# Optimization experiments

Hardware: AMD Instinct MI355X
Metric: run time of the kernel (lower is better)

Reference implementation:

```python
import jax, jax.numpy as jnp
import numpy as np

N_NODES = 10000
N_EDGES = 320000
HIDDEN = 16      # hidden_state_size
MSG = 64         # message_size
EDGE_FEAT = 32


def setup_inputs() -> dict:
    key = jax.random.key(0)
    ks = jax.random.split(key, 8)
    node_features = jax.random.normal(ks[0], (N_NODES, HIDDEN), dtype=jnp.float32)
    edge_features = jax.random.normal(ks[1], (N_EDGES, EDGE_FEAT), dtype=jnp.float32)
    edge_sources = jax.random.randint(ks[2], (N_EDGES,), 0, N_NODES, dtype=jnp.int32)
    edge_targets = jax.random.randint(ks[3], (N_EDGES,), 0, N_NODES, dtype=jnp.int32)
    hidden = jax.random.normal(ks[4], (N_NODES, HIDDEN), dtype=jnp.float32)
    initial = jax.random.normal(ks[5], (N_NODES, HIDDEN), dtype=jnp.float32)
    # Dense(edge_feat -> MSG*HIDDEN), glorot-ish scale
    W = jax.random.normal(ks[6], (EDGE_FEAT, MSG * HIDDEN), dtype=jnp.float32) / np.float32(np.sqrt(EDGE_FEAT))
    b = jnp.zeros((MSG * HIDDEN,), dtype=jnp.float32)
    return {
        "node_features": node_features,
        "edge_features": edge_features,
        "edge_sources": edge_sources,
        "edge_targets": edge_targets,
        "hidden": hidden,
        "initial": initial,
        "W": W,
        "b": b,
    }


def reference(node_features, edge_features, edge_sources, edge_targets, hidden, initial, W, b):
    # Per edge: edge_mat = Dense(edge_feat) reshaped (MSG, HIDDEN);
    # message = edge_mat @ hidden[source]; aggregate = sum over incoming edges per target node.
    num_nodes = node_features.shape[0]
    edge_mat = (edge_features @ W + b).reshape(-1, MSG, HIDDEN)  # [E, M, H]
    neigh = hidden[edge_sources]                                  # [E, H] gather
    messages = jnp.einsum("emh,eh->em", edge_mat, neigh)         # [E, M] batched matvec
    out = jax.ops.segment_sum(messages, edge_targets, num_segments=num_nodes)  # [N, M]
    return out
```

## Files before the change

### kernel.cpp

```cpp
#include <hip/hip_runtime.h>
#include <hip/hip_bf16.h>

#define N_NODES 10000
#define N_EDGES 320000
#define HIDDEN 16
#define MSG 64
#define EDGE_FEAT 32
#define KSTEPS 17
#define EPB 64

typedef __attribute__((ext_vector_type(2))) _Float16 f16x2;
typedef __attribute__((ext_vector_type(4))) _Float16 f16x4;
typedef __attribute__((ext_vector_type(8))) _Float16 f16x8;
typedef __attribute__((ext_vector_type(4))) float    f32x4;

union H8 { f16x8 v; f16x2 p[4]; f16x4 q[2]; };

__global__ void zero_prep(const float* __restrict__ W, const float* __restrict__ bias,
                          ushort* __restrict__ WrB, int* __restrict__ cnt,
                          float4* __restrict__ out4, int n4) {
    if (blockIdx.x < KSTEPS) {
        const int ks   = blockIdx.x;
        const int nt   = threadIdx.x >> 6;
        const int lane = threadIdx.x & 63;
        const int g    = lane >> 4;
        const int n    = nt * 16 + (lane & 15);
        ushort* dst = WrB + (((size_t)ks * 4 + nt) * 64 + lane) * 8;
        #pragma unroll
        for (int i = 0; i < 8; ++i) {
            const int k = ks * 32 + g * 8 + i;
            float v;
            if (k < 512)      v = W[(size_t)(k >> 4) * 1024 + n * 16 + (k & 15)];
            else if (k < 528) v = bias[n * 16 + (k - 512)];
            else              v = 0.0f;
            const _Float16 hv = (_Float16)v;
            dst[i] = *reinterpret_cast<const ushort*>(&hv);
        }
    } else if (blockIdx.x < KSTEPS + 40) {
        const int idx = (blockIdx.x - KSTEPS) * 256 + threadIdx.x;
        if (idx < N_NODES) cnt[idx] = 0;
    } else {
        const int i = (blockIdx.x - KSTEPS - 40) * 256 + threadIdx.x;
        if (i < n4) out4[i] = make_float4(0.f, 0.f, 0.f, 0.f);
    }
}

__global__ __launch_bounds__(256) void rank_kernel(const int* __restrict__ tgt,
                                                   int* __restrict__ cnt,
                                                   int* __restrict__ rank) {
    const int e = blockIdx.x * 256 + threadIdx.x;
    if (e < N_EDGES) rank[e] = atomicAdd(&cnt[tgt[e]], 1);
}

__global__ __launch_bounds__(1024) void scan_kernel(const int* __restrict__ cnt,
                                                    int* __restrict__ starts) {
    __shared__ int wsum[16];
    __shared__ int wbase[16];
    const int tid  = threadIdx.x;
    const int lane = tid & 63;
    const int wv   = tid >> 6;
    int c[10];
    int s = 0;
    #pragma unroll
    for (int j = 0; j < 10; ++j) {
        const int idx = tid * 10 + j;
        c[j] = (idx < N_NODES) ? cnt[idx] : 0;
        s += c[j];
    }
    int v = s;
    #pragma unroll
    for (int d = 1; d < 64; d <<= 1) {
        const int u = __shfl_up(v, d);
        if (lane >= d) v += u;
    }
    if (lane == 63) wsum[wv] = v;
    __syncthreads();
    if (tid < 16) {
        const int w = wsum[tid];
        int iv = w;
        #pragma unroll
        for (int d = 1; d < 16; d <<= 1) {
            const int u = __shfl_up(iv, d);
            if (tid >= d) iv += u;
        }
        wbase[tid] = iv - w;
    }
    __syncthreads();
    int running = wbase[wv] + (v - s);
    #pragma unroll
    for (int j = 0; j < 10; ++j) {
        const int idx = tid * 10 + j;
        if (idx < N_NODES) starts[idx] = running;
        running += c[j];
    }
    if (tid == 1023) starts[N_NODES] = N_EDGES;
}

__global__ __launch_bounds__(256) void build_desc(
    const int* __restrict__ tgt, const int* __restrict__ rank,
    const int* __restrict__ starts, const int* __restrict__ src,
    int4* __restrict__ edesc) {
    const int e = blockIdx.x * 256 + threadIdx.x;
    if (e < N_EDGES) {
        const int t = tgt[e];
        edesc[starts[t] + rank[e]] = make_int4(e, src[e], t, 0);
    }
}

__global__ __launch_bounds__(256, 8) void fused_msg(
    const int4*   __restrict__ edesc,
    const float*  __restrict__ ef,
    const float*  __restrict__ hidden,
    const ushort* __restrict__ WrB,
    float*        __restrict__ out)
{
    __shared__ _Float16 ef_h[EPB][36];
    __shared__ _Float16 nb_h[EPB][16];
    __shared__ int      tgt_s[EPB];
    __shared__ _Float16 msg_h[EPB][68];

    const int tid = threadIdx.x;
    const int s0  = blockIdx.x * EPB;

    {
        const int sl = tid >> 2;
        const int q  = tid & 3;
        const int4 d = edesc[s0 + sl];
        const int e  = d.x;
        const int sn = d.y;

        const float4* ep = (const float4*)(ef + (size_t)e * EDGE_FEAT + q * 8);
        const float4 v0 = ep[0], v1 = ep[1];
        _Float16* dst = &ef_h[sl][q * 8];
        *(f16x4*)(dst + 0) = f16x4{(_Float16)v0.x, (_Float16)v0.y, (_Float16)v0.z, (_Float16)v0.w};
        *(f16x4*)(dst + 4) = f16x4{(_Float16)v1.x, (_Float16)v1.y, (_Float16)v1.z, (_Float16)v1.w};

        const float4 h0 = *(const float4*)(hidden + (size_t)sn * HIDDEN + q * 4);
        *(f16x4*)&nb_h[sl][q * 4] =
            f16x4{(_Float16)h0.x, (_Float16)h0.y, (_Float16)h0.z, (_Float16)h0.w};

        if (q == 3) {
            ef_h[sl][32] = (_Float16)1.0f;
            ef_h[sl][33] = (_Float16)0.0f;
            ef_h[sl][34] = (_Float16)0.0f;
            ef_h[sl][35] = (_Float16)0.0f;
        } else if (q == 0) {
            tgt_s[sl] = d.z;
        }
    }
    __syncthreads();

    const int nt   = tid >> 6;
    const int lane = tid & 63;
    const int er   = lane & 15;
    const int g    = lane >> 4;
    const int hoff = (g & 1) * 8;
    const int fg   = g >> 1;

    H8 nb[4];
    #pragma unroll
    for (int rt = 0; rt < 4; ++rt)
        nb[rt].v = *(const f16x8*)&nb_h[rt * 16 + er][hoff];

    f32x4 acc[4];
    #pragma unroll
    for (int rt = 0; rt < 4; ++rt) acc[rt] = f32x4{0.f, 0.f, 0.f, 0.f};

    const f16x8* Bp = (const f16x8*)WrB;

    #pragma unroll
    for (int ks = 0; ks < KSTEPS; ++ks) {
        const f16x8 b = Bp[(ks * 4 + nt) * 64 + lane];
        #pragma unroll
        for (int rt = 0; rt < 4; ++rt) {
            const _Float16 a = ef_h[rt * 16 + er][2 * ks + fg];
            const f16x2 av = {a, a};
            H8 af;
            #pragma unroll
            for (int q = 0; q < 4; ++q) af.p[q] = av * nb[rt].p[q];
            acc[rt] = __builtin_amdgcn_mfma_f32_16x16x32_f16(af.v, b, acc[rt], 0, 0, 0);
        }
    }

    #pragma unroll
    for (int rt = 0; rt < 4; ++rt) {
        #pragma unroll
        for (int r = 0; r < 4; ++r) {
            msg_h[rt * 16 + g * 4 + r][nt * 16 + er] = (_Float16)acc[rt][r];
        }
    }
    __syncthreads();

    const int c = tid & 63;
    const int rbase = (tid >> 6) * 16;
    float run = (float)msg_h[rbase][c];
    int   cur = tgt_s[rbase];
    #pragma unroll
    for (int r = 1; r < 16; ++r) {
        const int   tg = tgt_s[rbase + r];
        const float m  = (float)msg_h[rbase + r][c];
        if (tg != cur) {
            atomicAdd(out + (size_t)cur * MSG + c, run);
            cur = tg;
            run = m;
        } else {
            run += m;
        }
    }
    atomicAdd(out + (size_t)cur * MSG + c, run);
}

__global__ __launch_bounds__(256) void zero_out(float* __restrict__ p, int n4) {
    const int i = blockIdx.x * 256 + threadIdx.x;
    if (i < n4) ((float4*)p)[i] = make_float4(0.f, 0.f, 0.f, 0.f);
}

__global__ __launch_bounds__(256, 4) void msg_mfma(
    const float* __restrict__ ef, const int* __restrict__ src,
    const int* __restrict__ tgt, const float* __restrict__ hidden,
    const ushort* __restrict__ WrB, float* __restrict__ out)
{
    __shared__ float ef_s[64][36];
    __shared__ float neigh_s[64][20];
    __shared__ int   tgt_s[64];
    const int tid = threadIdx.x;
    const int e0  = blockIdx.x * 64;
    {
        const int e = tid >> 2, h4 = (tid & 3) * 4;
        const int s = src[e0 + e];
        *(float4*)&neigh_s[e][h4] = *(const float4*)(hidden + (size_t)s * HIDDEN + h4);
    }
    {
        const int e = tid >> 2, f8 = (tid & 3) * 8;
        const float* p = ef + (size_t)(e0 + e) * EDGE_FEAT + f8;
        *(float4*)&ef_s[e][f8]     = *(const float4*)(p);
        *(float4*)&ef_s[e][f8 + 4] = *(const float4*)(p + 4);
    }
    if (tid < 64) { ef_s[tid][32] = 1.0f; ef_s[tid][33] = 0.0f; tgt_s[tid] = tgt[e0 + tid]; }
    __syncthreads();
    const int wave = tid >> 6, lane = tid & 63;
    const int er = lane & 15, g = lane >> 4;
    const int e_loc = wave * 16 + er;
    const int h0 = (g & 1) * 8, fg = g >> 1;
    float nb[8];
    #pragma unroll
    for (int j = 0; j < 8; ++j) nb[j] = neigh_s[e_loc][h0 + j];
    f32x4 acc0 = {0.f,0.f,0.f,0.f}, acc1 = acc0, acc2 = acc0, acc3 = acc0;
    const f16x8* Bp = (const f16x8*)WrB;
    #pragma unroll
    for (int ks = 0; ks < KSTEPS; ++ks) {
        const float a = ef_s[e_loc][2 * ks + fg];
        f16x8 af;
        #pragma unroll
        for (int j = 0; j < 8; ++j) af[j] = (_Float16)(a * nb[j]);
        const f16x8 b0 = Bp[(ks * 4 + 0) * 64 + lane];
        const f16x8 b1 = Bp[(ks * 4 + 1) * 64 + lane];
        const f16x8 b2 = Bp[(ks * 4 + 2) * 64 + lane];
        const f16x8 b3 = Bp[(ks * 4 + 3) * 64 + lane];
        acc0 = __builtin_amdgcn_mfma_f32_16x16x32_f16(af, b0, acc0, 0, 0, 0);
        acc1 = __builtin_amdgcn_mfma_f32_16x16x32_f16(af, b1, acc1, 0, 0, 0);
        acc2 = __builtin_amdgcn_mfma_f32_16x16x32_f16(af, b2, acc2, 0, 0, 0);
        acc3 = __builtin_amdgcn_mfma_f32_16x16x32_f16(af, b3, acc3, 0, 0, 0);
    }
    #pragma unroll
    for (int r = 0; r < 4; ++r) {
        const int t = tgt_s[wave * 16 + g * 4 + r];
        float* op = out + (size_t)t * MSG;
        atomicAdd(op +      er, acc0[r]);
        atomicAdd(op + 16 + er, acc1[r]);
        atomicAdd(op + 32 + er, acc2[r]);
        atomicAdd(op + 48 + er, acc3[r]);
    }
}

extern "C" void kernel_launch(void* const* d_in, const int* in_sizes, int n_in,
                              void* d_out, int out_size, void* d_ws, size_t ws_size,
                              hipStream_t stream) {
    const float* ef     = (const float*)d_in[1];
    const int*   src    = (const int*)d_in[2];
    const int*   tgt    = (const int*)d_in[3];
    const float* hidden = (const float*)d_in[4];
    const float* W      = (const float*)d_in[6];
    const float* bias   = (const float*)d_in[7];
    float* out = (float*)d_out;
    char*  ws  = (char*)d_ws;

    const size_t o_wrb    = 0;
    const size_t o_starts = 69632;
    const size_t o_cnt    = 109648;
    const size_t o_rank   = 149648;
    const size_t o_desc   = 1429648;
    const size_t need     = o_desc + (size_t)N_EDGES * 16;

    ushort* WrB = (ushort*)(ws + o_wrb);
    const int n4 = out_size / 4;

    if (ws_size >= need) {
        int*  starts = (int*)(ws + o_starts);
        int*  cnt    = (int*)(ws + o_cnt);
        int*  rank   = (int*)(ws + o_rank);
        int4* edesc  = (int4*)(ws + o_desc);

        const int zb_cnt = 40;
        const int zb_out = (n4 + 255) / 256;
        zero_prep<<<KSTEPS + zb_cnt + zb_out, 256, 0, stream>>>(W, bias, WrB, cnt,
                                                                (float4*)out, n4);
        rank_kernel<<<(N_EDGES + 255) / 256, 256, 0, stream>>>(tgt, cnt, rank);
        scan_kernel<<<1, 1024, 0, stream>>>(cnt, starts);
        build_desc<<<(N_EDGES + 255) / 256, 256, 0, stream>>>(tgt, rank, starts, src, edesc);
        fused_msg<<<N_EDGES / EPB, 256, 0, stream>>>(edesc, ef, hidden, WrB, out);
    } else {
        zero_prep<<<KSTEPS, 256, 0, stream>>>(W, bias, WrB, nullptr, nullptr, 0);
        zero_out<<<(n4 + 255) / 256, 256, 0, stream>>>(out, n4);
        msg_mfma<<<N_EDGES / 64, 256, 0, stream>>>(ef, src, tgt, hidden, WrB, out);
    }
}
```

Before: 75.68 us.

## Process two edge chunks per block with prefetch and 2x2 MFMA wave tiling

Each block of fused_msg now handles two 64-edge chunks, prefetching the next chunk's descriptors, edge features and hidden rows into registers while the current chunk computes and scatters. The MFMA work is retiled so each wave computes a 2x2 block of 16x16 tiles, which reuses the A fragments and B loads across two MFMAs each. The intent is to hide gather latency and cut redundant B-matrix loads per wave. In exchange there are half as many blocks, more registers per thread, and an extra barrier per chunk.

```diff
diff --git a/kernel.cpp b/kernel.cpp
--- a/kernel.cpp
+++ b/kernel.cpp
@@ -8,6 +8,7 @@
 #define EDGE_FEAT 32
 #define KSTEPS 17
 #define EPB 64
+#define NCHUNK 2
 
 typedef __attribute__((ext_vector_type(2))) _Float16 f16x2;
 typedef __attribute__((ext_vector_type(4))) _Float16 f16x4;
@@ -116,98 +117,114 @@
 {
     __shared__ _Float16 ef_h[EPB][36];
     __shared__ _Float16 nb_h[EPB][16];
-    __shared__ int      tgt_s[EPB];
+    __shared__ int      tgt_s[2][EPB];
     __shared__ _Float16 msg_h[EPB][68];
 
-    const int tid = threadIdx.x;
-    const int s0  = blockIdx.x * EPB;
-
-    {
-        const int sl = tid >> 2;
-        const int q  = tid & 3;
-        const int4 d = edesc[s0 + sl];
-        const int e  = d.x;
-        const int sn = d.y;
-
-        const float4* ep = (const float4*)(ef + (size_t)e * EDGE_FEAT + q * 8);
-        const float4 v0 = ep[0], v1 = ep[1];
-        _Float16* dst = &ef_h[sl][q * 8];
-        *(f16x4*)(dst + 0) = f16x4{(_Float16)v0.x, (_Float16)v0.y, (_Float16)v0.z, (_Float16)v0.w};
-        *(f16x4*)(dst + 4) = f16x4{(_Float16)v1.x, (_Float16)v1.y, (_Float16)v1.z, (_Float16)v1.w};
-
-        const float4 h0 = *(const float4*)(hidden + (size_t)sn * HIDDEN + q * 4);
-        *(f16x4*)&nb_h[sl][q * 4] =
-            f16x4{(_Float16)h0.x, (_Float16)h0.y, (_Float16)h0.z, (_Float16)h0.w};
-
-        if (q == 3) {
-            ef_h[sl][32] = (_Float16)1.0f;
-            ef_h[sl][33] = (_Float16)0.0f;
-            ef_h[sl][34] = (_Float16)0.0f;
-            ef_h[sl][35] = (_Float16)0.0f;
-        } else if (q == 0) {
-            tgt_s[sl] = d.z;
-        }
-    }
-    __syncthreads();
-
-    const int nt   = tid >> 6;
+    const int tid  = threadIdx.x;
+    const int sl   = tid >> 2;
+    const int q    = tid & 3;
+    const int base = blockIdx.x * (EPB * NCHUNK);
+
+    const int w    = tid >> 6;
+    const int wr   = w >> 1;
+    const int wc   = w & 1;
     const int lane = tid & 63;
     const int er   = lane & 15;
     const int g    = lane >> 4;
     const int hoff = (g & 1) * 8;
     const int fg   = g >> 1;
-
-    H8 nb[4];
-    #pragma unroll
-    for (int rt = 0; rt < 4; ++rt)
-        nb[rt].v = *(const f16x8*)&nb_h[rt * 16 + er][hoff];
-
-    f32x4 acc[4];
-    #pragma unroll
-    for (int rt = 0; rt < 4; ++rt) acc[rt] = f32x4{0.f, 0.f, 0.f, 0.f};
-
+    const int rt0 = wr * 2, rt1 = wr * 2 + 1;
+    const int ct0 = wc * 2, ct1 = wc * 2 + 1;
     const f16x8* Bp = (const f16x8*)WrB;
 
-    #pragma unroll
-    for (int ks = 0; ks < KSTEPS; ++ks) {
-        const f16x8 b = Bp[(ks * 4 + nt) * 64 + lane];
-        #pragma unroll
-        for (int rt = 0; rt < 4; ++rt) {
-            const _Float16 a = ef_h[rt * 16 + er][2 * ks + fg];
-            const f16x2 av = {a, a};
-            H8 af;
+    int4   d   = edesc[base + sl];
+    float4 pe0 = *(const float4*)(ef + (size_t)d.x * EDGE_FEAT + q * 8);
+    float4 pe1 = *(const float4*)(ef + (size_t)d.x * EDGE_FEAT + q * 8 + 4);
+    float4 ph  = *(const float4*)(hidden + (size_t)d.y * HIDDEN + q * 4);
+
+    #pragma unroll
+    for (int c = 0; c < NCHUNK; ++c) {
+        {
+            _Float16* dst = &ef_h[sl][q * 8];
+            *(f16x4*)(dst + 0) = f16x4{(_Float16)pe0.x, (_Float16)pe0.y,
+                                       (_Float16)pe0.z, (_Float16)pe0.w};
+            *(f16x4*)(dst + 4) = f16x4{(_Float16)pe1.x, (_Float16)pe1.y,
+                                       (_Float16)pe1.z, (_Float16)pe1.w};
+            *(f16x4*)&nb_h[sl][q * 4] = f16x4{(_Float16)ph.x, (_Float16)ph.y,
+                                              (_Float16)ph.z, (_Float16)ph.w};
+            if (q == 3) {
+                ef_h[sl][32] = (_Float16)1.0f;
+                ef_h[sl][33] = (_Float16)0.0f;
+                ef_h[sl][34] = (_Float16)0.0f;
+                ef_h[sl][35] = (_Float16)0.0f;
+            } else if (q == 0) {
+                tgt_s[c & 1][sl] = d.z;
+            }
+        }
+        __syncthreads();
+
+        if (c + 1 < NCHUNK) d = edesc[base + (c + 1) * EPB + sl];
+
+        H8 nb0, nb1;
+        nb0.v = *(const f16x8*)&nb_h[rt0 * 16 + er][hoff];
+        nb1.v = *(const f16x8*)&nb_h[rt1 * 16 + er][hoff];
+
+        f32x4 a00 = {0.f,0.f,0.f,0.f}, a01 = a00, a10 = a00, a11 = a00;
+        #pragma unroll
+        for (int ks = 0; ks < KSTEPS; ++ks) {
+            const f16x8 b0 = Bp[(ks * 4 + ct0) * 64 + lane];
+            const f16x8 b1 = Bp[(ks * 4 + ct1) * 64 + lane];
+            const _Float16 aa0 = ef_h[rt0 * 16 + er][2 * ks + fg];
+            const _Float16 aa1 = ef_h[rt1 * 16 + er][2 * ks + fg];
+            const f16x2 av0 = {aa0, aa0};
+            const f16x2 av1 = {aa1, aa1};
+            H8 af0, af1;
             #pragma unroll
-            for (int q = 0; q < 4; ++q) af.p[q] = av * nb[rt].p[q];
-            acc[rt] = __builtin_amdgcn_mfma_f32_16x16x32_f16(af.v, b, acc[rt], 0, 0, 0);
-        }
-    }
-
-    #pragma unroll
-    for (int rt = 0; rt < 4; ++rt) {
+            for (int p = 0; p < 4; ++p) {
+                af0.p[p] = av0 * nb0.p[p];
+                af1.p[p] = av1 * nb1.p[p];
+            }
+            a00 = __builtin_amdgcn_mfma_f32_16x16x32_f16(af0.v, b0, a00, 0, 0, 0);
+            a01 = __builtin_amdgcn_mfma_f32_16x16x32_f16(af0.v, b1, a01, 0, 0, 0);
+            a10 = __builtin_amdgcn_mfma_f32_16x16x32_f16(af1.v, b0, a10, 0, 0, 0);
+            a11 = __builtin_amdgcn_mfma_f32_16x16x32_f16(af1.v, b1, a11, 0, 0, 0);
+        }
+
         #pragma unroll
         for (int r = 0; r < 4; ++r) {
-            msg_h[rt * 16 + g * 4 + r][nt * 16 + er] = (_Float16)acc[rt][r];
-        }
-    }
-    __syncthreads();
-
-    const int c = tid & 63;
-    const int rbase = (tid >> 6) * 16;
-    float run = (float)msg_h[rbase][c];
-    int   cur = tgt_s[rbase];
-    #pragma unroll
-    for (int r = 1; r < 16; ++r) {
-        const int   tg = tgt_s[rbase + r];
-        const float m  = (float)msg_h[rbase + r][c];
-        if (tg != cur) {
-            atomicAdd(out + (size_t)cur * MSG + c, run);
-            cur = tg;
-            run = m;
-        } else {
-            run += m;
-        }
-    }
-    atomicAdd(out + (size_t)cur * MSG + c, run);
+            const int rowA = rt0 * 16 + g * 4 + r;
+            const int rowB = rt1 * 16 + g * 4 + r;
+            msg_h[rowA][ct0 * 16 + er] = (_Float16)a00[r];
+            msg_h[rowA][ct1 * 16 + er] = (_Float16)a01[r];
+            msg_h[rowB][ct0 * 16 + er] = (_Float16)a10[r];
+            msg_h[rowB][ct1 * 16 + er] = (_Float16)a11[r];
+        }
+        __syncthreads();
+
+        if (c + 1 < NCHUNK) {
+            pe0 = *(const float4*)(ef + (size_t)d.x * EDGE_FEAT + q * 8);
+            pe1 = *(const float4*)(ef + (size_t)d.x * EDGE_FEAT + q * 8 + 4);
+            ph  = *(const float4*)(hidden + (size_t)d.y * HIDDEN + q * 4);
+        }
+
+        const int cc    = tid & 63;
+        const int rbase = (tid >> 6) * 16;
+        float run = (float)msg_h[rbase][cc];
+        int   cur = tgt_s[c & 1][rbase];
+        #pragma unroll
+        for (int r = 1; r < 16; ++r) {
+            const int   tg = tgt_s[c & 1][rbase + r];
+            const float m  = (float)msg_h[rbase + r][cc];
+            if (tg != cur) {
+                atomicAdd(out + (size_t)cur * MSG + cc, run);
+                cur = tg;
+                run = m;
+            } else {
+                run += m;
+            }
+        }
+        atomicAdd(out + (size_t)cur * MSG + cc, run);
+    }
 }
 
 __global__ __launch_bounds__(256) void zero_out(float* __restrict__ p, int n4) {
@@ -308,7 +325,7 @@
         rank_kernel<<<(N_EDGES + 255) / 256, 256, 0, stream>>>(tgt, cnt, rank);
         scan_kernel<<<1, 1024, 0, stream>>>(cnt, starts);
         build_desc<<<(N_EDGES + 255) / 256, 256, 0, stream>>>(tgt, rank, starts, src, edesc);
-        fused_msg<<<N_EDGES / EPB, 256, 0, stream>>>(edesc, ef, hidden, WrB, out);
+        fused_msg<<<N_EDGES / (EPB * NCHUNK), 256, 0, stream>>>(edesc, ef, hidden, WrB, out);
     } else {
         zero_prep<<<KSTEPS, 256, 0, stream>>>(W, bias, WrB, nullptr, nullptr, 0);
         zero_out<<<(n4 + 255) / 256, 256, 0, stream>>>(out, n4);
```

Result: slower. 115.3 us (+52.3%).
